# Kernel optimization log

Hardware: AMD Instinct MI355X
Metric: run time of the kernel (lower is better)

## Reference

```python
import jax, jax.numpy as jnp
import numpy as np

B, T, C = 2, 2048, 2048
N_HEAD, N_KV = 16, 2
D_HEAD = C // N_HEAD          # 128
R = N_HEAD // N_KV            # q heads per kv head = 8


def setup_inputs() -> dict:
    key = jax.random.key(0)
    ks = jax.random.split(key, 5)
    s = 0.02
    return {
        "x": jax.random.normal(ks[0], (B, T, C), dtype=jnp.float32),
        "Wq": jax.random.normal(ks[1], (C, C), dtype=jnp.float32) * s,
        "Wk": jax.random.normal(ks[2], (C, N_KV * D_HEAD), dtype=jnp.float32) * s,
        "Wv": jax.random.normal(ks[3], (C, N_KV * D_HEAD), dtype=jnp.float32) * s,
        "Wo": jax.random.normal(ks[4], (C, C), dtype=jnp.float32) * s,
    }


def reference(x, Wq, Wk, Wv, Wo):
    b, t, c = x.shape
    # projections (no bias per config.bias=False)
    q = (x @ Wq).reshape(b, t, N_KV, R, D_HEAD)        # group q heads by kv group
    k = (x @ Wk).reshape(b, t, N_KV, D_HEAD)
    v = (x @ Wv).reshape(b, t, N_KV, D_HEAD)
    scale = 1.0 / jnp.sqrt(jnp.float32(D_HEAD))
    # scores: [b, g(kv), r, tq, tk] -- broadcast kv heads instead of repeat_interleave
    att = jnp.einsum('btgrd,bsgd->bgrts', q, k) * scale
    causal = jnp.tril(jnp.ones((t, t), dtype=bool))
    att = jnp.where(causal, att, -jnp.inf)
    att = jax.nn.softmax(att, axis=-1)
    y = jnp.einsum('bgrts,bsgd->btgrd', att, v).reshape(b, t, c)
    return y @ Wo
```

## Files before the change

kernel.cpp:

```cpp
#include <hip/hip_runtime.h>
#include <stdint.h>

using bf16x8 = __attribute__((ext_vector_type(8))) __bf16;
using f32x4  = __attribute__((ext_vector_type(4))) float;
using u32x4  = __attribute__((ext_vector_type(4))) unsigned;

#define GLL(g, l) __builtin_amdgcn_global_load_lds(                                  \
    (const __attribute__((address_space(1))) void*)(g),                              \
    (__attribute__((address_space(3))) void*)(l), 16, 0, 0)

__device__ __forceinline__ unsigned short f2bf(float f) {
  unsigned u = __builtin_bit_cast(unsigned, f);
  u += 0x7FFF + ((u >> 16) & 1);
  return (unsigned short)(u >> 16);
}
__device__ __forceinline__ float bf2f(unsigned short u) {
  unsigned v = ((unsigned)u) << 16;
  return __builtin_bit_cast(float, v);
}

__device__ __forceinline__ void tcast_block(const float* __restrict__ W,
                                            unsigned short* __restrict__ Wt,
                                            int K, int N, int kb, int nb,
                                            float (*T)[65], int t) {
  const int k0 = kb * 64, n0 = nb * 64;
  const int r4 = t >> 6, c = t & 63;
#pragma unroll
  for (int p = 0; p < 16; ++p) {
    int r = p * 4 + r4;
    T[r][c] = W[(size_t)(k0 + r) * N + n0 + c];
  }
  __syncthreads();
#pragma unroll
  for (int p = 0; p < 16; ++p) {
    int r = p * 4 + r4;
    Wt[(size_t)(n0 + r) * K + k0 + c] = f2bf(T[c][r]);
  }
}

__global__ __launch_bounds__(256) void prep_kernel(const float* __restrict__ x,
                                                   const float* __restrict__ Wq,
                                                   const float* __restrict__ Wk,
                                                   const float* __restrict__ Wv,
                                                   const float* __restrict__ Wo,
                                                   unsigned short* __restrict__ xb,
                                                   unsigned short* __restrict__ Wqkvt,
                                                   unsigned short* __restrict__ Wot) {
  __shared__ float T[64][65];
  int bid = blockIdx.x;
  const int t = threadIdx.x;
  if (bid < 8192) {
    int i = bid * 256 + t;
    float4 v = reinterpret_cast<const float4*>(x)[i];
    ushort4 o;
    o.x = f2bf(v.x); o.y = f2bf(v.y); o.z = f2bf(v.z); o.w = f2bf(v.w);
    reinterpret_cast<ushort4*>(xb)[i] = o;
    return;
  }
  bid -= 8192;
  if (bid < 1024) { tcast_block(Wq, Wqkvt, 2048, 2048, bid & 31, bid >> 5, T, t); return; }
  bid -= 1024;
  if (bid < 128)  { tcast_block(Wk, Wqkvt + (size_t)2048 * 2048, 2048, 256, bid & 31, bid >> 5, T, t); return; }
  bid -= 128;
  if (bid < 128)  { tcast_block(Wv, Wqkvt + (size_t)2304 * 2048, 2048, 256, bid & 31, bid >> 5, T, t); return; }
  bid -= 128;
  tcast_block(Wo, Wot, 2048, 2048, bid & 31, bid >> 5, T, t);
}

__global__ __launch_bounds__(256) void tv_kernel(const unsigned short* __restrict__ V,
                                                 unsigned short* __restrict__ Vt) {
  __shared__ unsigned short T[64][68];
  const int t0 = blockIdx.x * 64;
  const int d0 = blockIdx.y * 64;
  const int t = threadIdx.x;
  const int r4 = t >> 6, c = t & 63;
#pragma unroll
  for (int p = 0; p < 16; ++p) {
    int r = p * 4 + r4;
    T[r][c] = V[(size_t)(t0 + r) * 2560 + 2304 + d0 + c];
  }
  __syncthreads();
  const int b = t0 >> 11;
  const int tl = t0 & 2047;
#pragma unroll
  for (int p = 0; p < 16; ++p) {
    int dr = p * 4 + r4;
    int dg = d0 + dr;
    int g = dg >> 7, dl = dg & 127;
    Vt[(size_t)((b * 2 + g) * 128 + dl) * 2048 + tl + c] = T[c][dr];
  }
}

template <bool FP32OUT>
__global__ __launch_bounds__(256) void gemm_bt_kernel(const unsigned short* __restrict__ A,
                                                      const unsigned short* __restrict__ Bt,
                                                      void* __restrict__ Cout,
                                                      int K, int lda, int ldb, int ldc,
                                                      float scale, int nscale) {
  __shared__ __align__(16) unsigned short As[128 * 64];
  __shared__ __align__(16) unsigned short Bs[128 * 64];
  const int m0 = blockIdx.x * 128, n0 = blockIdx.y * 128;
  const int t = threadIdx.x;
  const int w = t >> 6, lane = t & 63;
  const int l15 = lane & 15, quad = lane >> 4;
  const int wm = (w >> 1) * 64, wn = (w & 1) * 64;

  const int srow = lane >> 3;
  const int sgl = (lane & 7) ^ srow;

  f32x4 acc[4][4] = {};

  for (int k0 = 0; k0 < K; k0 += 64) {
    __syncthreads();
#pragma unroll
    for (int p = 0; p < 4; ++p) {
      int rowbase = p * 32 + w * 8;
      GLL(&A[(size_t)(m0 + rowbase + srow) * lda + k0 + sgl * 8], &As[rowbase * 64]);
      GLL(&Bt[(size_t)(n0 + rowbase + srow) * ldb + k0 + sgl * 8], &Bs[rowbase * 64]);
    }
    __syncthreads();
#pragma unroll
    for (int kk = 0; kk < 64; kk += 32) {
      const int kg = kk >> 3;
      const int phys = ((kg + quad) ^ (l15 & 7)) * 8;
      bf16x8 af[4], bfr[4];
#pragma unroll
      for (int mt = 0; mt < 4; ++mt)
        af[mt] = *reinterpret_cast<const bf16x8*>(&As[(wm + mt * 16 + l15) * 64 + phys]);
#pragma unroll
      for (int nt = 0; nt < 4; ++nt)
        bfr[nt] = *reinterpret_cast<const bf16x8*>(&Bs[(wn + nt * 16 + l15) * 64 + phys]);
#pragma unroll
      for (int mt = 0; mt < 4; ++mt)
#pragma unroll
        for (int nt = 0; nt < 4; ++nt)
          acc[mt][nt] = __builtin_amdgcn_mfma_f32_16x16x32_bf16(af[mt], bfr[nt], acc[mt][nt], 0, 0, 0);
    }
  }

  const float sc = (n0 < nscale) ? scale : 1.0f;
#pragma unroll
  for (int mt = 0; mt < 4; ++mt) {
#pragma unroll
    for (int reg = 0; reg < 4; ++reg) {
      int row = m0 + wm + mt * 16 + quad * 4 + reg;
#pragma unroll
      for (int nt = 0; nt < 4; ++nt) {
        int col = n0 + wn + nt * 16 + l15;
        float v = acc[mt][nt][reg] * sc;
        if (FP32OUT)
          reinterpret_cast<float*>(Cout)[(size_t)row * ldc + col] = v;
        else
          reinterpret_cast<unsigned short*>(Cout)[(size_t)row * ldc + col] = f2bf(v);
      }
    }
  }
}

#define LDQK 2560
__global__ __launch_bounds__(256, 2) void attn_kernel(const unsigned short* __restrict__ Q,
                                                      const unsigned short* __restrict__ Kg,
                                                      const unsigned short* __restrict__ Vt,
                                                      float* __restrict__ O0,
                                                      unsigned short* __restrict__ O1,
                                                      float* __restrict__ L) {
  __shared__ __align__(16) unsigned short Ks[2][64 * 128];
  __shared__ __align__(16) unsigned short Vs[2][128 * 64];

  const int s  = blockIdx.x;
  const int bx = blockIdx.y;
  const int hh = blockIdx.z & 15;
  const int b  = blockIdx.z >> 4;
  const int g  = hh >> 3;
  const int t  = threadIdx.x;
  const int wg = t >> 6, lane = t & 63;
  const int l15 = lane & 15, quad = lane >> 4;

  const unsigned short* Kbase = Kg + (size_t)b * 2048 * LDQK + g * 128;
  const unsigned short* Vbase = Vt + (size_t)(b * 2 + g) * 128 * 2048;

  const int k_r = lane >> 4;
  const int v_r = lane >> 3;

  auto issueK = [&](int tile, unsigned short* dst) {
    const unsigned short* kb = Kbase + (size_t)(tile * 64) * LDQK;
#pragma unroll
    for (int p = 0; p < 4; ++p) {
      int rowbase = p * 16 + wg * 4;
      int row = rowbase + k_r;
      int gl = (lane & 15) ^ (row & 15);
      GLL(&kb[(size_t)row * LDQK + gl * 8], &dst[rowbase * 128]);
    }
  };
  auto issueV = [&](int tile, unsigned short* dst) {
    const unsigned short* vb = Vbase + tile * 64;
#pragma unroll
    for (int p = 0; p < 4; ++p) {
      int rowbase = p * 32 + wg * 8;
      int row = rowbase + v_r;
      int gl = (lane & 7) ^ (row & 7);
      GLL(&vb[(size_t)row * 2048 + gl * 8], &dst[rowbase * 64]);
    }
  };

  int pb = 0;
  issueK(s, Ks[0]);
  issueV(s, Vs[0]);

  for (int ph = 0; ph < 2; ++ph) {
    const int iq = ph ? (15 - bx) : bx;

    bf16x8 qf[2][4];
#pragma unroll
    for (int mi = 0; mi < 2; ++mi) {
      int qrow = iq * 128 + wg * 32 + mi * 16 + l15;
      const unsigned short* qp = &Q[(size_t)(b * 2048 + qrow) * LDQK + hh * 128 + quad * 8];
#pragma unroll
      for (int dk = 0; dk < 4; ++dk)
        qf[mi][dk] = *reinterpret_cast<const bf16x8*>(qp + dk * 32);
    }

    f32x4 o[2][8] = {};
    float l_run[2] = {};

    for (int j = 0; j <= iq; ++j) {
      const int tile = 2 * j + s;
      __syncthreads();
      const int cur = pb, nxt = pb ^ 1;

      if (j < iq) {
        issueK(tile + 2, Ks[nxt]);
        issueV(tile + 2, Vs[nxt]);
      } else if (ph == 0) {
        issueK(s, Ks[nxt]);
        issueV(s, Vs[nxt]);
      }

      f32x4 sc[2][4] = {};
      __builtin_amdgcn_s_setprio(1);
#pragma unroll
      for (int nt = 0; nt < 4; ++nt) {
#pragma unroll
        for (int dk = 0; dk < 4; ++dk) {
          int phys = (dk * 4 + quad) ^ l15;
          bf16x8 kf = *reinterpret_cast<const bf16x8*>(&Ks[cur][(nt * 16 + l15) * 128 + phys * 8]);
          sc[0][nt] = __builtin_amdgcn_mfma_f32_16x16x32_bf16(kf, qf[0][dk], sc[0][nt], 0, 0, 0);
          sc[1][nt] = __builtin_amdgcn_mfma_f32_16x16x32_bf16(kf, qf[1][dk], sc[1][nt], 0, 0, 0);
        }
      }
      __builtin_amdgcn_s_setprio(0);
      if (j == iq) {
#pragma unroll
        for (int mi = 0; mi < 2; ++mi)
#pragma unroll
          for (int nt = 0; nt < 4; ++nt) {
#pragma unroll
            for (int reg = 0; reg < 4; ++reg) {
              int kcol = tile * 64 + nt * 16 + quad * 4 + reg;
              int qr = iq * 128 + wg * 32 + mi * 16 + l15;
              if (kcol > qr) sc[mi][nt][reg] = -1e30f;
            }
          }
      }

#pragma unroll
      for (int kk = 0; kk < 2; ++kk) {
        bf16x8 pf[2];
#pragma unroll
        for (int mi = 0; mi < 2; ++mi) {
          float pe[4], po[4];
#pragma unroll
          for (int reg = 0; reg < 4; ++reg) {
            pe[reg] = __builtin_exp2f(__builtin_fmaf(sc[mi][kk * 2 + 0][reg], 1.44269504f, -23.08312064f));
            po[reg] = __builtin_exp2f(__builtin_fmaf(sc[mi][kk * 2 + 1][reg], 1.44269504f, -23.08312064f));
            l_run[mi] += pe[reg] + po[reg];
          }
          unsigned a0, a1, b0, b1;
          asm("v_cvt_pk_bf16_f32 %0, %1, %2" : "=v"(a0) : "v"(pe[0]), "v"(pe[1]));
          asm("v_cvt_pk_bf16_f32 %0, %1, %2" : "=v"(a1) : "v"(pe[2]), "v"(pe[3]));
          asm("v_cvt_pk_bf16_f32 %0, %1, %2" : "=v"(b0) : "v"(po[0]), "v"(po[1]));
          asm("v_cvt_pk_bf16_f32 %0, %1, %2" : "=v"(b1) : "v"(po[2]), "v"(po[3]));
          asm("v_permlane32_swap_b32 %0, %1" : "+v"(a0), "+v"(b0));
          asm("v_permlane16_swap_b32 %0, %1" : "+v"(a0), "+v"(b0));
          asm("v_permlane32_swap_b32 %0, %1" : "+v"(a1), "+v"(b1));
          asm("v_permlane16_swap_b32 %0, %1" : "+v"(a1), "+v"(b1));
          u32x4 w;
          w[0] = a0;
          w[1] = a1;
          w[2] = b0;
          w[3] = b1;
          pf[mi] = __builtin_bit_cast(bf16x8, w);
        }
        __builtin_amdgcn_s_setprio(1);
#pragma unroll
        for (int dt = 0; dt < 8; ++dt) {
          int phys = ((kk * 4 + quad) ^ (l15 & 7));
          bf16x8 vf = *reinterpret_cast<const bf16x8*>(&Vs[cur][(dt * 16 + l15) * 64 + phys * 8]);
          o[0][dt] = __builtin_amdgcn_mfma_f32_16x16x32_bf16(pf[0], vf, o[0][dt], 0, 0, 0);
          o[1][dt] = __builtin_amdgcn_mfma_f32_16x16x32_bf16(pf[1], vf, o[1][dt], 0, 0, 0);
        }
        __builtin_amdgcn_s_setprio(0);
      }
      pb ^= 1;
    }

#pragma unroll
    for (int mi = 0; mi < 2; ++mi) {
      l_run[mi] += __shfl_xor(l_run[mi], 16);
      l_run[mi] += __shfl_xor(l_run[mi], 32);
    }

#pragma unroll
    for (int mi = 0; mi < 2; ++mi) {
      if (quad == 0) {
        int lrow = wg * 32 + mi * 16 + l15;
        L[(size_t)s * 65536 + (size_t)(b * 2048 + iq * 128 + lrow) * 16 + hh] = l_run[mi];
      }
#pragma unroll
      for (int reg = 0; reg < 4; ++reg) {
        int row = wg * 32 + mi * 16 + quad * 4 + reg;
        size_t base = (size_t)(b * 2048 + iq * 128 + row) * 2048 + hh * 128;
        if (s == 0) {
#pragma unroll
          for (int dt = 0; dt < 8; ++dt)
            O0[base + dt * 16 + l15] = o[mi][dt][reg];
        } else {
#pragma unroll
          for (int dt = 0; dt < 8; ++dt)
            O1[base + dt * 16 + l15] = f2bf(o[mi][dt][reg]);
        }
      }
    }
  }
}

__global__ __launch_bounds__(256) void merge_kernel(const float* __restrict__ O0,
                                                    unsigned short* __restrict__ O1,
                                                    const float* __restrict__ L) {
  int i4 = blockIdx.x * 256 + threadIdx.x;
  int e = i4 << 2;
  int tr = e >> 11;
  int hh = (e >> 7) & 15;
  float l = L[tr * 16 + hh] + L[65536 + tr * 16 + hh];
  float inv = 1.0f / l;
  float4 a = reinterpret_cast<const float4*>(O0)[i4];
  ushort4 u = reinterpret_cast<const ushort4*>(O1)[i4];
  ushort4 r;
  r.x = f2bf((a.x + bf2f(u.x)) * inv);
  r.y = f2bf((a.y + bf2f(u.y)) * inv);
  r.z = f2bf((a.z + bf2f(u.z)) * inv);
  r.w = f2bf((a.w + bf2f(u.w)) * inv);
  reinterpret_cast<ushort4*>(O1)[i4] = r;
}

extern "C" void kernel_launch(void* const* d_in, const int* in_sizes, int n_in,
                              void* d_out, int out_size, void* d_ws, size_t ws_size,
                              hipStream_t stream) {
  const float* x  = (const float*)d_in[0];
  const float* Wq = (const float*)d_in[1];
  const float* Wk = (const float*)d_in[2];
  const float* Wv = (const float*)d_in[3];
  const float* Wo = (const float*)d_in[4];

  char* ws = (char*)d_ws;
  unsigned short* xb    = (unsigned short*)(ws + 0);
  unsigned short* Wqkvt = (unsigned short*)(ws + 16777216);
  unsigned short* Wot   = (unsigned short*)(ws + 27262976);
  unsigned short* QKVb  = (unsigned short*)(ws + 35651584);
  unsigned short* Vtb   = (unsigned short*)(ws + 56623104);
  float*          Lb    = (float*)(ws + 58720256);
  unsigned short* Yb    = xb;

  prep_kernel<<<10496, 256, 0, stream>>>(x, Wq, Wk, Wv, Wo, xb, Wqkvt, Wot);

  const float qscale = 0.08838834764831845f;
  gemm_bt_kernel<false><<<dim3(32, 20), 256, 0, stream>>>(xb, Wqkvt, QKVb,
                                                          2048, 2048, 2048, 2560, qscale, 2048);
  tv_kernel<<<dim3(64, 4), 256, 0, stream>>>(QKVb, Vtb);
  attn_kernel<<<dim3(2, 8, 32), 256, 0, stream>>>(QKVb, QKVb + 2048, Vtb,
                                                  (float*)d_out, Yb, Lb);
  merge_kernel<<<8192, 256, 0, stream>>>((const float*)d_out, Yb, Lb);
  gemm_bt_kernel<true><<<dim3(32, 16), 256, 0, stream>>>(Yb, Wot, d_out,
                                                         2048, 2048, 2048, 2048, 1.0f, 0);
}
```

Measured before the change: 278.7 us.

## Split attention block over eight waves with one 16-row Q tile per wave

The attention kernel now runs 512 threads (8 waves) per block instead of 256. Each wave owns 16 query rows instead of 32, which halves its accumulator and score registers and lets more waves stay resident under the new launch bounds. K/V tile loads are spread across the eight waves with fewer loads each, and the s_setprio hints are removed. The cost is that each K/V fragment read from LDS now feeds one MFMA instead of two, doubling LDS read traffic per unit of compute.

```diff
diff --git a/kernel.cpp b/kernel.cpp
--- a/kernel.cpp
+++ b/kernel.cpp
@@ -158,7 +158,7 @@
 }
 
 #define LDQK 2560
-__global__ __launch_bounds__(256, 2) void attn_kernel(const unsigned short* __restrict__ Q,
+__global__ __launch_bounds__(512, 4) void attn_kernel(const unsigned short* __restrict__ Q,
                                                       const unsigned short* __restrict__ Kg,
                                                       const unsigned short* __restrict__ Vt,
                                                       float* __restrict__ O0,
@@ -185,8 +185,8 @@
   auto issueK = [&](int tile, unsigned short* dst) {
     const unsigned short* kb = Kbase + (size_t)(tile * 64) * LDQK;
 #pragma unroll
-    for (int p = 0; p < 4; ++p) {
-      int rowbase = p * 16 + wg * 4;
+    for (int p = 0; p < 2; ++p) {
+      int rowbase = p * 32 + wg * 4;
       int row = rowbase + k_r;
       int gl = (lane & 15) ^ (row & 15);
       GLL(&kb[(size_t)row * LDQK + gl * 8], &dst[rowbase * 128]);
@@ -195,8 +195,8 @@
   auto issueV = [&](int tile, unsigned short* dst) {
     const unsigned short* vb = Vbase + tile * 64;
 #pragma unroll
-    for (int p = 0; p < 4; ++p) {
-      int rowbase = p * 32 + wg * 8;
+    for (int p = 0; p < 2; ++p) {
+      int rowbase = p * 64 + wg * 8;
       int row = rowbase + v_r;
       int gl = (lane & 7) ^ (row & 7);
       GLL(&vb[(size_t)row * 2048 + gl * 8], &dst[rowbase * 64]);
@@ -210,18 +210,17 @@
   for (int ph = 0; ph < 2; ++ph) {
     const int iq = ph ? (15 - bx) : bx;
 
-    bf16x8 qf[2][4];
-#pragma unroll
-    for (int mi = 0; mi < 2; ++mi) {
-      int qrow = iq * 128 + wg * 32 + mi * 16 + l15;
+    bf16x8 qf[4];
+    {
+      int qrow = iq * 128 + wg * 16 + l15;
       const unsigned short* qp = &Q[(size_t)(b * 2048 + qrow) * LDQK + hh * 128 + quad * 8];
 #pragma unroll
       for (int dk = 0; dk < 4; ++dk)
-        qf[mi][dk] = *reinterpret_cast<const bf16x8*>(qp + dk * 32);
-    }
-
-    f32x4 o[2][8] = {};
-    float l_run[2] = {};
+        qf[dk] = *reinterpret_cast<const bf16x8*>(qp + dk * 32);
+    }
+
+    f32x4 o[8] = {};
+    float l_run = 0.0f;
 
     for (int j = 0; j <= iq; ++j) {
       const int tile = 2 * j + s;
@@ -236,44 +235,38 @@
         issueV(s, Vs[nxt]);
       }
 
-      f32x4 sc[2][4] = {};
-      __builtin_amdgcn_s_setprio(1);
+      f32x4 sc[4] = {};
 #pragma unroll
       for (int nt = 0; nt < 4; ++nt) {
 #pragma unroll
         for (int dk = 0; dk < 4; ++dk) {
           int phys = (dk * 4 + quad) ^ l15;
           bf16x8 kf = *reinterpret_cast<const bf16x8*>(&Ks[cur][(nt * 16 + l15) * 128 + phys * 8]);
-          sc[0][nt] = __builtin_amdgcn_mfma_f32_16x16x32_bf16(kf, qf[0][dk], sc[0][nt], 0, 0, 0);
-          sc[1][nt] = __builtin_amdgcn_mfma_f32_16x16x32_bf16(kf, qf[1][dk], sc[1][nt], 0, 0, 0);
+          sc[nt] = __builtin_amdgcn_mfma_f32_16x16x32_bf16(kf, qf[dk], sc[nt], 0, 0, 0);
         }
       }
-      __builtin_amdgcn_s_setprio(0);
       if (j == iq) {
 #pragma unroll
-        for (int mi = 0; mi < 2; ++mi)
-#pragma unroll
-          for (int nt = 0; nt < 4; ++nt) {
-#pragma unroll
-            for (int reg = 0; reg < 4; ++reg) {
-              int kcol = tile * 64 + nt * 16 + quad * 4 + reg;
-              int qr = iq * 128 + wg * 32 + mi * 16 + l15;
-              if (kcol > qr) sc[mi][nt][reg] = -1e30f;
-            }
+        for (int nt = 0; nt < 4; ++nt) {
+#pragma unroll
+          for (int reg = 0; reg < 4; ++reg) {
+            int kcol = tile * 64 + nt * 16 + quad * 4 + reg;
+            int qr = iq * 128 + wg * 16 + l15;
+            if (kcol > qr) sc[nt][reg] = -1e30f;
           }
+        }
       }
 
 #pragma unroll
       for (int kk = 0; kk < 2; ++kk) {
-        bf16x8 pf[2];
-#pragma unroll
-        for (int mi = 0; mi < 2; ++mi) {
+        bf16x8 pf;
+        {
           float pe[4], po[4];
 #pragma unroll
           for (int reg = 0; reg < 4; ++reg) {
-            pe[reg] = __builtin_exp2f(__builtin_fmaf(sc[mi][kk * 2 + 0][reg], 1.44269504f, -23.08312064f));
-            po[reg] = __builtin_exp2f(__builtin_fmaf(sc[mi][kk * 2 + 1][reg], 1.44269504f, -23.08312064f));
-            l_run[mi] += pe[reg] + po[reg];
+            pe[reg] = __builtin_exp2f(__builtin_fmaf(sc[kk * 2 + 0][reg], 1.44269504f, -23.08312064f));
+            po[reg] = __builtin_exp2f(__builtin_fmaf(sc[kk * 2 + 1][reg], 1.44269504f, -23.08312064f));
+            l_run += pe[reg] + po[reg];
           }
           unsigned a0, a1, b0, b1;
           asm("v_cvt_pk_bf16_f32 %0, %1, %2" : "=v"(a0) : "v"(pe[0]), "v"(pe[1]));
@@ -289,46 +282,37 @@
           w[1] = a1;
           w[2] = b0;
           w[3] = b1;
-          pf[mi] = __builtin_bit_cast(bf16x8, w);
+          pf = __builtin_bit_cast(bf16x8, w);
         }
-        __builtin_amdgcn_s_setprio(1);
 #pragma unroll
         for (int dt = 0; dt < 8; ++dt) {
           int phys = ((kk * 4 + quad) ^ (l15 & 7));
           bf16x8 vf = *reinterpret_cast<const bf16x8*>(&Vs[cur][(dt * 16 + l15) * 64 + phys * 8]);
-          o[0][dt] = __builtin_amdgcn_mfma_f32_16x16x32_bf16(pf[0], vf, o[0][dt], 0, 0, 0);
-          o[1][dt] = __builtin_amdgcn_mfma_f32_16x16x32_bf16(pf[1], vf, o[1][dt], 0, 0, 0);
+          o[dt] = __builtin_amdgcn_mfma_f32_16x16x32_bf16(pf, vf, o[dt], 0, 0, 0);
         }
-        __builtin_amdgcn_s_setprio(0);
       }
       pb ^= 1;
     }
 
-#pragma unroll
-    for (int mi = 0; mi < 2; ++mi) {
-      l_run[mi] += __shfl_xor(l_run[mi], 16);
-      l_run[mi] += __shfl_xor(l_run[mi], 32);
-    }
-
-#pragma unroll
-    for (int mi = 0; mi < 2; ++mi) {
-      if (quad == 0) {
-        int lrow = wg * 32 + mi * 16 + l15;
-        L[(size_t)s * 65536 + (size_t)(b * 2048 + iq * 128 + lrow) * 16 + hh] = l_run[mi];
-      }
-#pragma unroll
-      for (int reg = 0; reg < 4; ++reg) {
-        int row = wg * 32 + mi * 16 + quad * 4 + reg;
-        size_t base = (size_t)(b * 2048 + iq * 128 + row) * 2048 + hh * 128;
-        if (s == 0) {
-#pragma unroll
-          for (int dt = 0; dt < 8; ++dt)
-            O0[base + dt * 16 + l15] = o[mi][dt][reg];
-        } else {
-#pragma unroll
-          for (int dt = 0; dt < 8; ++dt)
-            O1[base + dt * 16 + l15] = f2bf(o[mi][dt][reg]);
-        }
+    l_run += __shfl_xor(l_run, 16);
+    l_run += __shfl_xor(l_run, 32);
+
+    if (quad == 0) {
+      int lrow = wg * 16 + l15;
+      L[(size_t)s * 65536 + (size_t)(b * 2048 + iq * 128 + lrow) * 16 + hh] = l_run;
+    }
+#pragma unroll
+    for (int reg = 0; reg < 4; ++reg) {
+      int row = wg * 16 + quad * 4 + reg;
+      size_t base = (size_t)(b * 2048 + iq * 128 + row) * 2048 + hh * 128;
+      if (s == 0) {
+#pragma unroll
+        for (int dt = 0; dt < 8; ++dt)
+          O0[base + dt * 16 + l15] = o[dt][reg];
+      } else {
+#pragma unroll
+        for (int dt = 0; dt < 8; ++dt)
+          O1[base + dt * 16 + l15] = f2bf(o[dt][reg]);
       }
     }
   }
@@ -377,7 +361,7 @@
   gemm_bt_kernel<false><<<dim3(32, 20), 256, 0, stream>>>(xb, Wqkvt, QKVb,
                                                           2048, 2048, 2048, 2560, qscale, 2048);
   tv_kernel<<<dim3(64, 4), 256, 0, stream>>>(QKVb, Vtb);
-  attn_kernel<<<dim3(2, 8, 32), 256, 0, stream>>>(QKVb, QKVb + 2048, Vtb,
+  attn_kernel<<<dim3(2, 8, 32), 512, 0, stream>>>(QKVb, QKVb + 2048, Vtb,
                                                   (float*)d_out, Yb, Lb);
   merge_kernel<<<8192, 256, 0, stream>>>((const float*)d_out, Yb, Lb);
   gemm_bt_kernel<true><<<dim3(32, 16), 256, 0, stream>>>(Yb, Wot, d_out,
```

After: 273.1 us. -2.0%, faster.

## Drop split-K attention and merge kernel; one block per query tile

Applied to the files above, without the earlier changes.

Replaces the two-way key split (each block handling even or odd key tiles for a pair of query tiles, followed by a merge kernel) with one block per query tile that walks all key tiles and normalises in-register before writing bf16 output. This removes the fp32 partial output writes, the L buffer and the separate merge pass. The grid is linearised with heavy tiles scheduled first. Blocks now have unequal work (no balanced pairing), and the setprio hints are removed.

```diff
diff --git a/kernel.cpp b/kernel.cpp
--- a/kernel.cpp
+++ b/kernel.cpp
@@ -161,16 +161,17 @@
 __global__ __launch_bounds__(256, 2) void attn_kernel(const unsigned short* __restrict__ Q,
                                                       const unsigned short* __restrict__ Kg,
                                                       const unsigned short* __restrict__ Vt,
-                                                      float* __restrict__ O0,
-                                                      unsigned short* __restrict__ O1,
-                                                      float* __restrict__ L) {
+                                                      unsigned short* __restrict__ Y) {
   __shared__ __align__(16) unsigned short Ks[2][64 * 128];
   __shared__ __align__(16) unsigned short Vs[2][128 * 64];
 
-  const int s  = blockIdx.x;
-  const int bx = blockIdx.y;
-  const int hh = blockIdx.z & 15;
-  const int b  = blockIdx.z >> 4;
+  const int w  = blockIdx.x;
+  const int hq = w >> 8;
+  const int z  = (w >> 3) & 31;
+  const int q8 = w & 7;
+  const int iq = hq ? q8 : 15 - q8;
+  const int hh = z & 15;
+  const int b  = z >> 4;
   const int g  = hh >> 3;
   const int t  = threadIdx.x;
   const int wg = t >> 6, lane = t & 63;
@@ -204,153 +205,117 @@
   };
 
   int pb = 0;
-  issueK(s, Ks[0]);
-  issueV(s, Vs[0]);
-
-  for (int ph = 0; ph < 2; ++ph) {
-    const int iq = ph ? (15 - bx) : bx;
-
-    bf16x8 qf[2][4];
-#pragma unroll
-    for (int mi = 0; mi < 2; ++mi) {
-      int qrow = iq * 128 + wg * 32 + mi * 16 + l15;
-      const unsigned short* qp = &Q[(size_t)(b * 2048 + qrow) * LDQK + hh * 128 + quad * 8];
-#pragma unroll
-      for (int dk = 0; dk < 4; ++dk)
-        qf[mi][dk] = *reinterpret_cast<const bf16x8*>(qp + dk * 32);
-    }
-
-    f32x4 o[2][8] = {};
-    float l_run[2] = {};
-
-    for (int j = 0; j <= iq; ++j) {
-      const int tile = 2 * j + s;
-      __syncthreads();
-      const int cur = pb, nxt = pb ^ 1;
-
-      if (j < iq) {
-        issueK(tile + 2, Ks[nxt]);
-        issueV(tile + 2, Vs[nxt]);
-      } else if (ph == 0) {
-        issueK(s, Ks[nxt]);
-        issueV(s, Vs[nxt]);
+  issueK(0, Ks[0]);
+  issueV(0, Vs[0]);
+
+  bf16x8 qf[2][4];
+#pragma unroll
+  for (int mi = 0; mi < 2; ++mi) {
+    int qrow = iq * 128 + wg * 32 + mi * 16 + l15;
+    const unsigned short* qp = &Q[(size_t)(b * 2048 + qrow) * LDQK + hh * 128 + quad * 8];
+#pragma unroll
+    for (int dk = 0; dk < 4; ++dk)
+      qf[mi][dk] = *reinterpret_cast<const bf16x8*>(qp + dk * 32);
+  }
+
+  f32x4 o[2][8] = {};
+  float l_run[2] = {};
+  const int jlast = 2 * iq + 1;
+
+  for (int j = 0; j <= jlast; ++j) {
+    __syncthreads();
+    const int cur = pb, nxt = pb ^ 1;
+
+    if (j < jlast) {
+      issueK(j + 1, Ks[nxt]);
+      issueV(j + 1, Vs[nxt]);
+    }
+
+    f32x4 sc[2][4] = {};
+#pragma unroll
+    for (int nt = 0; nt < 4; ++nt) {
+#pragma unroll
+      for (int dk = 0; dk < 4; ++dk) {
+        int phys = (dk * 4 + quad) ^ l15;
+        bf16x8 kf = *reinterpret_cast<const bf16x8*>(&Ks[cur][(nt * 16 + l15) * 128 + phys * 8]);
+        sc[0][nt] = __builtin_amdgcn_mfma_f32_16x16x32_bf16(kf, qf[0][dk], sc[0][nt], 0, 0, 0);
+        sc[1][nt] = __builtin_amdgcn_mfma_f32_16x16x32_bf16(kf, qf[1][dk], sc[1][nt], 0, 0, 0);
       }
-
-      f32x4 sc[2][4] = {};
-      __builtin_amdgcn_s_setprio(1);
-#pragma unroll
-      for (int nt = 0; nt < 4; ++nt) {
-#pragma unroll
-        for (int dk = 0; dk < 4; ++dk) {
-          int phys = (dk * 4 + quad) ^ l15;
-          bf16x8 kf = *reinterpret_cast<const bf16x8*>(&Ks[cur][(nt * 16 + l15) * 128 + phys * 8]);
-          sc[0][nt] = __builtin_amdgcn_mfma_f32_16x16x32_bf16(kf, qf[0][dk], sc[0][nt], 0, 0, 0);
-          sc[1][nt] = __builtin_amdgcn_mfma_f32_16x16x32_bf16(kf, qf[1][dk], sc[1][nt], 0, 0, 0);
+    }
+    if (j >= jlast - 1) {
+#pragma unroll
+      for (int mi = 0; mi < 2; ++mi)
+#pragma unroll
+        for (int nt = 0; nt < 4; ++nt) {
+#pragma unroll
+          for (int reg = 0; reg < 4; ++reg) {
+            int kcol = j * 64 + nt * 16 + quad * 4 + reg;
+            int qr = iq * 128 + wg * 32 + mi * 16 + l15;
+            if (kcol > qr) sc[mi][nt][reg] = -1e30f;
+          }
         }
+    }
+
+#pragma unroll
+    for (int kk = 0; kk < 2; ++kk) {
+      bf16x8 pf[2];
+#pragma unroll
+      for (int mi = 0; mi < 2; ++mi) {
+        float pe[4], po[4];
+#pragma unroll
+        for (int reg = 0; reg < 4; ++reg) {
+          pe[reg] = __builtin_exp2f(__builtin_fmaf(sc[mi][kk * 2 + 0][reg], 1.44269504f, -23.08312064f));
+          po[reg] = __builtin_exp2f(__builtin_fmaf(sc[mi][kk * 2 + 1][reg], 1.44269504f, -23.08312064f));
+          l_run[mi] += pe[reg] + po[reg];
+        }
+        unsigned a0, a1, b0, b1;
+        asm("v_cvt_pk_bf16_f32 %0, %1, %2" : "=v"(a0) : "v"(pe[0]), "v"(pe[1]));
+        asm("v_cvt_pk_bf16_f32 %0, %1, %2" : "=v"(a1) : "v"(pe[2]), "v"(pe[3]));
+        asm("v_cvt_pk_bf16_f32 %0, %1, %2" : "=v"(b0) : "v"(po[0]), "v"(po[1]));
+        asm("v_cvt_pk_bf16_f32 %0, %1, %2" : "=v"(b1) : "v"(po[2]), "v"(po[3]));
+        asm("v_permlane32_swap_b32 %0, %1" : "+v"(a0), "+v"(b0));
+        asm("v_permlane16_swap_b32 %0, %1" : "+v"(a0), "+v"(b0));
+        asm("v_permlane32_swap_b32 %0, %1" : "+v"(a1), "+v"(b1));
+        asm("v_permlane16_swap_b32 %0, %1" : "+v"(a1), "+v"(b1));
+        u32x4 wd;
+        wd[0] = a0;
+        wd[1] = a1;
+        wd[2] = b0;
+        wd[3] = b1;
+        pf[mi] = __builtin_bit_cast(bf16x8, wd);
       }
-      __builtin_amdgcn_s_setprio(0);
-      if (j == iq) {
-#pragma unroll
-        for (int mi = 0; mi < 2; ++mi)
-#pragma unroll
-          for (int nt = 0; nt < 4; ++nt) {
-#pragma unroll
-            for (int reg = 0; reg < 4; ++reg) {
-              int kcol = tile * 64 + nt * 16 + quad * 4 + reg;
-              int qr = iq * 128 + wg * 32 + mi * 16 + l15;
-              if (kcol > qr) sc[mi][nt][reg] = -1e30f;
-            }
-          }
+#pragma unroll
+      for (int dt = 0; dt < 8; ++dt) {
+        int phys = ((kk * 4 + quad) ^ (l15 & 7));
+        bf16x8 vf = *reinterpret_cast<const bf16x8*>(&Vs[cur][(dt * 16 + l15) * 64 + phys * 8]);
+        o[0][dt] = __builtin_amdgcn_mfma_f32_16x16x32_bf16(pf[0], vf, o[0][dt], 0, 0, 0);
+        o[1][dt] = __builtin_amdgcn_mfma_f32_16x16x32_bf16(pf[1], vf, o[1][dt], 0, 0, 0);
       }
-
-#pragma unroll
-      for (int kk = 0; kk < 2; ++kk) {
-        bf16x8 pf[2];
-#pragma unroll
-        for (int mi = 0; mi < 2; ++mi) {
-          float pe[4], po[4];
-#pragma unroll
-          for (int reg = 0; reg < 4; ++reg) {
-            pe[reg] = __builtin_exp2f(__builtin_fmaf(sc[mi][kk * 2 + 0][reg], 1.44269504f, -23.08312064f));
-            po[reg] = __builtin_exp2f(__builtin_fmaf(sc[mi][kk * 2 + 1][reg], 1.44269504f, -23.08312064f));
-            l_run[mi] += pe[reg] + po[reg];
-          }
-          unsigned a0, a1, b0, b1;
-          asm("v_cvt_pk_bf16_f32 %0, %1, %2" : "=v"(a0) : "v"(pe[0]), "v"(pe[1]));
-          asm("v_cvt_pk_bf16_f32 %0, %1, %2" : "=v"(a1) : "v"(pe[2]), "v"(pe[3]));
-          asm("v_cvt_pk_bf16_f32 %0, %1, %2" : "=v"(b0) : "v"(po[0]), "v"(po[1]));
-          asm("v_cvt_pk_bf16_f32 %0, %1, %2" : "=v"(b1) : "v"(po[2]), "v"(po[3]));
-          asm("v_permlane32_swap_b32 %0, %1" : "+v"(a0), "+v"(b0));
-          asm("v_permlane16_swap_b32 %0, %1" : "+v"(a0), "+v"(b0));
-          asm("v_permlane32_swap_b32 %0, %1" : "+v"(a1), "+v"(b1));
-          asm("v_permlane16_swap_b32 %0, %1" : "+v"(a1), "+v"(b1));
-          u32x4 w;
-          w[0] = a0;
-          w[1] = a1;
-          w[2] = b0;
-          w[3] = b1;
-          pf[mi] = __builtin_bit_cast(bf16x8, w);
-        }
-        __builtin_amdgcn_s_setprio(1);
-#pragma unroll
-        for (int dt = 0; dt < 8; ++dt) {
-          int phys = ((kk * 4 + quad) ^ (l15 & 7));
-          bf16x8 vf = *reinterpret_cast<const bf16x8*>(&Vs[cur][(dt * 16 + l15) * 64 + phys * 8]);
-          o[0][dt] = __builtin_amdgcn_mfma_f32_16x16x32_bf16(pf[0], vf, o[0][dt], 0, 0, 0);
-          o[1][dt] = __builtin_amdgcn_mfma_f32_16x16x32_bf16(pf[1], vf, o[1][dt], 0, 0, 0);
-        }
-        __builtin_amdgcn_s_setprio(0);
-      }
-      pb ^= 1;
-    }
-
-#pragma unroll
-    for (int mi = 0; mi < 2; ++mi) {
-      l_run[mi] += __shfl_xor(l_run[mi], 16);
-      l_run[mi] += __shfl_xor(l_run[mi], 32);
-    }
-
-#pragma unroll
-    for (int mi = 0; mi < 2; ++mi) {
-      if (quad == 0) {
-        int lrow = wg * 32 + mi * 16 + l15;
-        L[(size_t)s * 65536 + (size_t)(b * 2048 + iq * 128 + lrow) * 16 + hh] = l_run[mi];
-      }
-#pragma unroll
-      for (int reg = 0; reg < 4; ++reg) {
-        int row = wg * 32 + mi * 16 + quad * 4 + reg;
-        size_t base = (size_t)(b * 2048 + iq * 128 + row) * 2048 + hh * 128;
-        if (s == 0) {
-#pragma unroll
-          for (int dt = 0; dt < 8; ++dt)
-            O0[base + dt * 16 + l15] = o[mi][dt][reg];
-        } else {
-#pragma unroll
-          for (int dt = 0; dt < 8; ++dt)
-            O1[base + dt * 16 + l15] = f2bf(o[mi][dt][reg]);
-        }
-      }
-    }
-  }
-}
-
-__global__ __launch_bounds__(256) void merge_kernel(const float* __restrict__ O0,
-                                                    unsigned short* __restrict__ O1,
-                                                    const float* __restrict__ L) {
-  int i4 = blockIdx.x * 256 + threadIdx.x;
-  int e = i4 << 2;
-  int tr = e >> 11;
-  int hh = (e >> 7) & 15;
-  float l = L[tr * 16 + hh] + L[65536 + tr * 16 + hh];
-  float inv = 1.0f / l;
-  float4 a = reinterpret_cast<const float4*>(O0)[i4];
-  ushort4 u = reinterpret_cast<const ushort4*>(O1)[i4];
-  ushort4 r;
-  r.x = f2bf((a.x + bf2f(u.x)) * inv);
-  r.y = f2bf((a.y + bf2f(u.y)) * inv);
-  r.z = f2bf((a.z + bf2f(u.z)) * inv);
-  r.w = f2bf((a.w + bf2f(u.w)) * inv);
-  reinterpret_cast<ushort4*>(O1)[i4] = r;
+    }
+    pb ^= 1;
+  }
+
+#pragma unroll
+  for (int mi = 0; mi < 2; ++mi) {
+    l_run[mi] += __shfl_xor(l_run[mi], 16);
+    l_run[mi] += __shfl_xor(l_run[mi], 32);
+  }
+
+#pragma unroll
+  for (int mi = 0; mi < 2; ++mi) {
+    float inv[4];
+#pragma unroll
+    for (int reg = 0; reg < 4; ++reg)
+      inv[reg] = 1.0f / __shfl(l_run[mi], quad * 4 + reg);
+#pragma unroll
+    for (int reg = 0; reg < 4; ++reg) {
+      int row = wg * 32 + mi * 16 + quad * 4 + reg;
+      size_t base = (size_t)(b * 2048 + iq * 128 + row) * 2048 + hh * 128;
+#pragma unroll
+      for (int dt = 0; dt < 8; ++dt)
+        Y[base + dt * 16 + l15] = f2bf(o[mi][dt][reg] * inv[reg]);
+    }
+  }
 }
 
 extern "C" void kernel_launch(void* const* d_in, const int* in_sizes, int n_in,
@@ -368,7 +333,6 @@
   unsigned short* Wot   = (unsigned short*)(ws + 27262976);
   unsigned short* QKVb  = (unsigned short*)(ws + 35651584);
   unsigned short* Vtb   = (unsigned short*)(ws + 56623104);
-  float*          Lb    = (float*)(ws + 58720256);
   unsigned short* Yb    = xb;
 
   prep_kernel<<<10496, 256, 0, stream>>>(x, Wq, Wk, Wv, Wo, xb, Wqkvt, Wot);
@@ -377,9 +341,7 @@
   gemm_bt_kernel<false><<<dim3(32, 20), 256, 0, stream>>>(xb, Wqkvt, QKVb,
                                                           2048, 2048, 2048, 2560, qscale, 2048);
   tv_kernel<<<dim3(64, 4), 256, 0, stream>>>(QKVb, Vtb);
-  attn_kernel<<<dim3(2, 8, 32), 256, 0, stream>>>(QKVb, QKVb + 2048, Vtb,
-                                                  (float*)d_out, Yb, Lb);
-  merge_kernel<<<8192, 256, 0, stream>>>((const float*)d_out, Yb, Lb);
+  attn_kernel<<<512, 256, 0, stream>>>(QKVb, QKVb + 2048, Vtb, Yb);
   gemm_bt_kernel<true><<<dim3(32, 16), 256, 0, stream>>>(Yb, Wot, d_out,
                                                          2048, 2048, 2048, 2048, 1.0f, 0);
 }
```

Result: no change. 278.4 us (-0.1%).

## Fuse all stages into one persistent kernel with software grid barriers

Applied to the files above, without the earlier changes.

Replaces six separate launches (prep, QKV GEMM, V transpose, attention, merge, output GEMM) with one persistent 512-block kernel. The stages are separated by an atomic-counter grid barrier, and the shared-memory layouts are unioned. This removes per-launch overhead and the gaps between kernels. In exchange, stages with few work units (the 640-tile GEMM, the 256-unit transpose) leave blocks idle or unevenly loaded. Co-residency of all 512 blocks is also assumed, which deadlocks if they cannot all run at once. The setprio hints in attention were also removed.

```diff
diff --git a/kernel.cpp b/kernel.cpp
--- a/kernel.cpp
+++ b/kernel.cpp
@@ -19,10 +19,40 @@
   return __builtin_bit_cast(float, v);
 }
 
-__device__ __forceinline__ void tcast_block(const float* __restrict__ W,
-                                            unsigned short* __restrict__ Wt,
-                                            int K, int N, int kb, int nb,
-                                            float (*T)[65], int t) {
+struct SMAttn { unsigned short Ks[2][64 * 128]; unsigned short Vs[2][128 * 64]; };
+struct SMGemm { unsigned short As[128 * 64]; unsigned short Bs[128 * 64]; };
+union SMem {
+  SMAttn a;
+  SMGemm g;
+  float T[64][65];
+  unsigned short Tv[64][68];
+};
+
+__device__ __forceinline__ void gridbar(unsigned* bar) {
+  __syncthreads();
+  if (threadIdx.x == 0) {
+    __threadfence();
+    unsigned* cnt = bar;
+    unsigned* gen = bar + 1;
+    unsigned g = __hip_atomic_load(gen, __ATOMIC_RELAXED, __HIP_MEMORY_SCOPE_AGENT);
+    unsigned a = __hip_atomic_fetch_add(cnt, 1u, __ATOMIC_ACQ_REL, __HIP_MEMORY_SCOPE_AGENT);
+    if (a == 511u) {
+      __hip_atomic_store(cnt, 0u, __ATOMIC_RELAXED, __HIP_MEMORY_SCOPE_AGENT);
+      __hip_atomic_fetch_add(gen, 1u, __ATOMIC_ACQ_REL, __HIP_MEMORY_SCOPE_AGENT);
+    } else {
+      while (__hip_atomic_load(gen, __ATOMIC_ACQUIRE, __HIP_MEMORY_SCOPE_AGENT) == g)
+        __builtin_amdgcn_s_sleep(2);
+    }
+  }
+  __syncthreads();
+  __threadfence();
+}
+
+__device__ __forceinline__ void tcast_unit(const float* __restrict__ W,
+                                           unsigned short* __restrict__ Wt,
+                                           int K, int N, int kb, int nb,
+                                           float (*T)[65]) {
+  const int t = threadIdx.x;
   const int k0 = kb * 64, n0 = nb * 64;
   const int r4 = t >> 6, c = t & 63;
 #pragma unroll
@@ -36,42 +66,12 @@
     int r = p * 4 + r4;
     Wt[(size_t)(n0 + r) * K + k0 + c] = f2bf(T[c][r]);
   }
-}
-
-__global__ __launch_bounds__(256) void prep_kernel(const float* __restrict__ x,
-                                                   const float* __restrict__ Wq,
-                                                   const float* __restrict__ Wk,
-                                                   const float* __restrict__ Wv,
-                                                   const float* __restrict__ Wo,
-                                                   unsigned short* __restrict__ xb,
-                                                   unsigned short* __restrict__ Wqkvt,
-                                                   unsigned short* __restrict__ Wot) {
-  __shared__ float T[64][65];
-  int bid = blockIdx.x;
-  const int t = threadIdx.x;
-  if (bid < 8192) {
-    int i = bid * 256 + t;
-    float4 v = reinterpret_cast<const float4*>(x)[i];
-    ushort4 o;
-    o.x = f2bf(v.x); o.y = f2bf(v.y); o.z = f2bf(v.z); o.w = f2bf(v.w);
-    reinterpret_cast<ushort4*>(xb)[i] = o;
-    return;
-  }
-  bid -= 8192;
-  if (bid < 1024) { tcast_block(Wq, Wqkvt, 2048, 2048, bid & 31, bid >> 5, T, t); return; }
-  bid -= 1024;
-  if (bid < 128)  { tcast_block(Wk, Wqkvt + (size_t)2048 * 2048, 2048, 256, bid & 31, bid >> 5, T, t); return; }
-  bid -= 128;
-  if (bid < 128)  { tcast_block(Wv, Wqkvt + (size_t)2304 * 2048, 2048, 256, bid & 31, bid >> 5, T, t); return; }
-  bid -= 128;
-  tcast_block(Wo, Wot, 2048, 2048, bid & 31, bid >> 5, T, t);
-}
-
-__global__ __launch_bounds__(256) void tv_kernel(const unsigned short* __restrict__ V,
-                                                 unsigned short* __restrict__ Vt) {
-  __shared__ unsigned short T[64][68];
-  const int t0 = blockIdx.x * 64;
-  const int d0 = blockIdx.y * 64;
+  __syncthreads();
+}
+
+__device__ __forceinline__ void tv_unit(const unsigned short* __restrict__ V,
+                                        unsigned short* __restrict__ Vt,
+                                        int t0, int d0, unsigned short (*T)[68]) {
   const int t = threadIdx.x;
   const int r4 = t >> 6, c = t & 63;
 #pragma unroll
@@ -89,17 +89,16 @@
     int g = dg >> 7, dl = dg & 127;
     Vt[(size_t)((b * 2 + g) * 128 + dl) * 2048 + tl + c] = T[c][dr];
   }
+  __syncthreads();
 }
 
 template <bool FP32OUT>
-__global__ __launch_bounds__(256) void gemm_bt_kernel(const unsigned short* __restrict__ A,
-                                                      const unsigned short* __restrict__ Bt,
-                                                      void* __restrict__ Cout,
-                                                      int K, int lda, int ldb, int ldc,
-                                                      float scale, int nscale) {
-  __shared__ __align__(16) unsigned short As[128 * 64];
-  __shared__ __align__(16) unsigned short Bs[128 * 64];
-  const int m0 = blockIdx.x * 128, n0 = blockIdx.y * 128;
+__device__ __forceinline__ void gemm_unit(const unsigned short* __restrict__ A,
+                                          const unsigned short* __restrict__ Bt,
+                                          void* __restrict__ Cout,
+                                          int m0, int n0, int K, int lda, int ldb, int ldc,
+                                          float scale, int nscale,
+                                          unsigned short* As, unsigned short* Bs) {
   const int t = threadIdx.x;
   const int w = t >> 6, lane = t & 63;
   const int l15 = lane & 15, quad = lane >> 4;
@@ -155,22 +154,19 @@
       }
     }
   }
+  __syncthreads();
 }
 
 #define LDQK 2560
-__global__ __launch_bounds__(256, 2) void attn_kernel(const unsigned short* __restrict__ Q,
-                                                      const unsigned short* __restrict__ Kg,
-                                                      const unsigned short* __restrict__ Vt,
-                                                      float* __restrict__ O0,
-                                                      unsigned short* __restrict__ O1,
-                                                      float* __restrict__ L) {
-  __shared__ __align__(16) unsigned short Ks[2][64 * 128];
-  __shared__ __align__(16) unsigned short Vs[2][128 * 64];
-
-  const int s  = blockIdx.x;
-  const int bx = blockIdx.y;
-  const int hh = blockIdx.z & 15;
-  const int b  = blockIdx.z >> 4;
+__device__ __forceinline__ void attn_unit(const unsigned short* __restrict__ Q,
+                                          const unsigned short* __restrict__ Kg,
+                                          const unsigned short* __restrict__ Vt,
+                                          float* __restrict__ O0,
+                                          unsigned short* __restrict__ O1,
+                                          float* __restrict__ L,
+                                          int s, int bx, int bh, SMAttn* sm) {
+  const int hh = bh & 15;
+  const int b  = bh >> 4;
   const int g  = hh >> 3;
   const int t  = threadIdx.x;
   const int wg = t >> 6, lane = t & 63;
@@ -204,8 +200,8 @@
   };
 
   int pb = 0;
-  issueK(s, Ks[0]);
-  issueV(s, Vs[0]);
+  issueK(s, sm->Ks[0]);
+  issueV(s, sm->Vs[0]);
 
   for (int ph = 0; ph < 2; ++ph) {
     const int iq = ph ? (15 - bx) : bx;
@@ -229,26 +225,24 @@
       const int cur = pb, nxt = pb ^ 1;
 
       if (j < iq) {
-        issueK(tile + 2, Ks[nxt]);
-        issueV(tile + 2, Vs[nxt]);
+        issueK(tile + 2, sm->Ks[nxt]);
+        issueV(tile + 2, sm->Vs[nxt]);
       } else if (ph == 0) {
-        issueK(s, Ks[nxt]);
-        issueV(s, Vs[nxt]);
+        issueK(s, sm->Ks[nxt]);
+        issueV(s, sm->Vs[nxt]);
       }
 
       f32x4 sc[2][4] = {};
-      __builtin_amdgcn_s_setprio(1);
 #pragma unroll
       for (int nt = 0; nt < 4; ++nt) {
 #pragma unroll
         for (int dk = 0; dk < 4; ++dk) {
           int phys = (dk * 4 + quad) ^ l15;
-          bf16x8 kf = *reinterpret_cast<const bf16x8*>(&Ks[cur][(nt * 16 + l15) * 128 + phys * 8]);
+          bf16x8 kf = *reinterpret_cast<const bf16x8*>(&sm->Ks[cur][(nt * 16 + l15) * 128 + phys * 8]);
           sc[0][nt] = __builtin_amdgcn_mfma_f32_16x16x32_bf16(kf, qf[0][dk], sc[0][nt], 0, 0, 0);
           sc[1][nt] = __builtin_amdgcn_mfma_f32_16x16x32_bf16(kf, qf[1][dk], sc[1][nt], 0, 0, 0);
         }
       }
-      __builtin_amdgcn_s_setprio(0);
       if (j == iq) {
 #pragma unroll
         for (int mi = 0; mi < 2; ++mi)
@@ -284,22 +278,20 @@
           asm("v_permlane16_swap_b32 %0, %1" : "+v"(a0), "+v"(b0));
           asm("v_permlane32_swap_b32 %0, %1" : "+v"(a1), "+v"(b1));
           asm("v_permlane16_swap_b32 %0, %1" : "+v"(a1), "+v"(b1));
-          u32x4 w;
-          w[0] = a0;
-          w[1] = a1;
-          w[2] = b0;
-          w[3] = b1;
-          pf[mi] = __builtin_bit_cast(bf16x8, w);
+          u32x4 wd;
+          wd[0] = a0;
+          wd[1] = a1;
+          wd[2] = b0;
+          wd[3] = b1;
+          pf[mi] = __builtin_bit_cast(bf16x8, wd);
         }
-        __builtin_amdgcn_s_setprio(1);
 #pragma unroll
         for (int dt = 0; dt < 8; ++dt) {
           int phys = ((kk * 4 + quad) ^ (l15 & 7));
-          bf16x8 vf = *reinterpret_cast<const bf16x8*>(&Vs[cur][(dt * 16 + l15) * 64 + phys * 8]);
+          bf16x8 vf = *reinterpret_cast<const bf16x8*>(&sm->Vs[cur][(dt * 16 + l15) * 64 + phys * 8]);
           o[0][dt] = __builtin_amdgcn_mfma_f32_16x16x32_bf16(pf[0], vf, o[0][dt], 0, 0, 0);
           o[1][dt] = __builtin_amdgcn_mfma_f32_16x16x32_bf16(pf[1], vf, o[1][dt], 0, 0, 0);
         }
-        __builtin_amdgcn_s_setprio(0);
       }
       pb ^= 1;
     }
@@ -332,12 +324,12 @@
       }
     }
   }
-}
-
-__global__ __launch_bounds__(256) void merge_kernel(const float* __restrict__ O0,
-                                                    unsigned short* __restrict__ O1,
-                                                    const float* __restrict__ L) {
-  int i4 = blockIdx.x * 256 + threadIdx.x;
+  __syncthreads();
+}
+
+__device__ __forceinline__ void merge_unit(const float* __restrict__ O0,
+                                           unsigned short* __restrict__ O1,
+                                           const float* __restrict__ L, int i4) {
   int e = i4 << 2;
   int tr = e >> 11;
   int hh = (e >> 7) & 15;
@@ -353,6 +345,63 @@
   reinterpret_cast<ushort4*>(O1)[i4] = r;
 }
 
+__global__ __launch_bounds__(256, 2) void mega_kernel(const float* __restrict__ x,
+                                                      const float* __restrict__ Wq,
+                                                      const float* __restrict__ Wk,
+                                                      const float* __restrict__ Wv,
+                                                      const float* __restrict__ Wo,
+                                                      unsigned short* __restrict__ xb,
+                                                      unsigned short* __restrict__ Wqkvt,
+                                                      unsigned short* __restrict__ Wot,
+                                                      unsigned short* __restrict__ QKVb,
+                                                      unsigned short* __restrict__ Vtb,
+                                                      float* __restrict__ O0s,
+                                                      unsigned short* __restrict__ Yb,
+                                                      float* __restrict__ Lb,
+                                                      float* __restrict__ outp,
+                                                      unsigned* __restrict__ bar) {
+  __shared__ __align__(16) SMem sm;
+  const int bid = blockIdx.x;
+  const int t = threadIdx.x;
+  const float qscale = 0.08838834764831845f;
+
+  for (int u = bid; u < 10496; u += 512) {
+    if (u < 8192) {
+      int i = u * 256 + t;
+      float4 v = reinterpret_cast<const float4*>(x)[i];
+      ushort4 o;
+      o.x = f2bf(v.x); o.y = f2bf(v.y); o.z = f2bf(v.z); o.w = f2bf(v.w);
+      reinterpret_cast<ushort4*>(xb)[i] = o;
+    } else {
+      int v2 = u - 8192;
+      if (v2 < 1024)       tcast_unit(Wq, Wqkvt, 2048, 2048, v2 & 31, v2 >> 5, sm.T);
+      else if (v2 < 1152) { int v3 = v2 - 1024; tcast_unit(Wk, Wqkvt + (size_t)2048 * 2048, 2048, 256, v3 & 31, v3 >> 5, sm.T); }
+      else if (v2 < 1280) { int v3 = v2 - 1152; tcast_unit(Wv, Wqkvt + (size_t)2304 * 2048, 2048, 256, v3 & 31, v3 >> 5, sm.T); }
+      else                { int v3 = v2 - 1280; tcast_unit(Wo, Wot, 2048, 2048, v3 & 31, v3 >> 5, sm.T); }
+    }
+  }
+  gridbar(bar);
+
+  for (int u = bid; u < 640; u += 512)
+    gemm_unit<false>(xb, Wqkvt, QKVb, (u & 31) * 128, (u >> 5) * 128,
+                     2048, 2048, 2048, 2560, qscale, 2048, sm.g.As, sm.g.Bs);
+  gridbar(bar);
+
+  for (int u = bid; u < 256; u += 512)
+    tv_unit(QKVb, Vtb, (u & 63) * 64, (u >> 6) * 64, sm.Tv);
+  gridbar(bar);
+
+  attn_unit(QKVb, QKVb + 2048, Vtb, O0s, Yb, Lb, bid & 1, (bid >> 1) & 7, bid >> 4, &sm.a);
+  gridbar(bar);
+
+  for (int u = bid; u < 8192; u += 512)
+    merge_unit(O0s, Yb, Lb, u * 256 + t);
+  gridbar(bar);
+
+  gemm_unit<true>(Yb, Wot, outp, (bid & 31) * 128, (bid >> 5) * 128,
+                  2048, 2048, 2048, 2048, 1.0f, 0, sm.g.As, sm.g.Bs);
+}
+
 extern "C" void kernel_launch(void* const* d_in, const int* in_sizes, int n_in,
                               void* d_out, int out_size, void* d_ws, size_t ws_size,
                               hipStream_t stream) {
@@ -369,17 +418,11 @@
   unsigned short* QKVb  = (unsigned short*)(ws + 35651584);
   unsigned short* Vtb   = (unsigned short*)(ws + 56623104);
   float*          Lb    = (float*)(ws + 58720256);
+  unsigned*       bar   = (unsigned*)(ws + 59244544);
   unsigned short* Yb    = xb;
 
-  prep_kernel<<<10496, 256, 0, stream>>>(x, Wq, Wk, Wv, Wo, xb, Wqkvt, Wot);
-
-  const float qscale = 0.08838834764831845f;
-  gemm_bt_kernel<false><<<dim3(32, 20), 256, 0, stream>>>(xb, Wqkvt, QKVb,
-                                                          2048, 2048, 2048, 2560, qscale, 2048);
-  tv_kernel<<<dim3(64, 4), 256, 0, stream>>>(QKVb, Vtb);
-  attn_kernel<<<dim3(2, 8, 32), 256, 0, stream>>>(QKVb, QKVb + 2048, Vtb,
-                                                  (float*)d_out, Yb, Lb);
-  merge_kernel<<<8192, 256, 0, stream>>>((const float*)d_out, Yb, Lb);
-  gemm_bt_kernel<true><<<dim3(32, 16), 256, 0, stream>>>(Yb, Wot, d_out,
-                                                         2048, 2048, 2048, 2048, 1.0f, 0);
-}
+  hipMemsetAsync(bar, 0, 8, stream);
+  mega_kernel<<<512, 256, 0, stream>>>(x, Wq, Wk, Wv, Wo, xb, Wqkvt, Wot,
+                                       QKVb, Vtb, (float*)d_out, Yb, Lb,
+                                       (float*)d_out, bar);
+}
```

Measured after the change: 1.018 ms. 265% more time.
